# Kernel optimization log

Measured on AMD Instinct MI355X. Metric: run time of the kernel, lower is better.

Reference implementation:

```python
import jax, jax.numpy as jnp
import numpy as np

RES = 64            # resolution -> RES*RES grid points
BW = 0.3            # kernel bandwidth
P = 2.0             # weight power
BOX = np.array([[-3.0, 3.0], [-3.0, 3.0]], dtype=np.float32)  # fixed_box [[min,max],[min,max]]


def _grid():
    # regular RES x RES grid over BOX, flattened to (M, 2)
    ax0 = np.linspace(BOX[0, 0], BOX[0, 1], RES, dtype=np.float32)
    ax1 = np.linspace(BOX[1, 0], BOX[1, 1], RES, dtype=np.float32)
    g0, g1 = np.meshgrid(ax0, ax1, indexing='ij')
    return jnp.asarray(np.stack([g0.ravel(), g1.ravel()], axis=-1))


def setup_inputs() -> dict:
    key = jax.random.key(0)
    k1, k2 = jax.random.split(key)
    Bs = jax.random.normal(k1, (4, 128, 16, 2), dtype=jnp.float32)  # birth corners (S,N,nB,2)
    Ds = jax.random.normal(k2, (4, 128, 16, 2), dtype=jnp.float32)  # death corners (S,N,nD,2)
    return {"Bs": Bs, "Ds": Ds}


def reference(Bs, Ds):
    # Bs: (S,N,nB,2) birth corners (pad with +inf), Ds: (S,N,nD,2) death corners (pad with -inf)
    x = _grid()                      # (M,2) grid points, M = RES*RES
    x0, x1 = x[:, 0], x[:, 1]

    # --- interleaving weights: dI0 per interval ---
    # pairwise relu(D - B).min(coords) -> max over (nB,nD); inf -> 0
    pw = jnp.min(jax.nn.relu(Ds[:, :, None, :, :] - Bs[:, :, :, None, :]), axis=-1)  # (S,N,nB,nD)
    w = jnp.max(pw, axis=(-1, -2))                                                   # (S,N)
    w = jnp.where(jnp.isfinite(w), w, 0.0)

    # --- distance from grid points to intervals ---
    # birth: min_k max_d (B[k,d] - x[d]); computed as elementwise max of the 2 coords
    db = jnp.min(
        jnp.maximum(Bs[..., 0][:, :, None, :] - x0[None, None, :, None],
                    Bs[..., 1][:, :, None, :] - x1[None, None, :, None]),
        axis=-1)                                                                     # (S,N,M)
    # death: min_k max_d (x[d] - D[k,d])
    dd = jnp.min(
        jnp.maximum(x0[None, None, :, None] - Ds[..., 0][:, :, None, :],
                    x1[None, None, :, None] - Ds[..., 1][:, :, None, :]),
        axis=-1)                                                                     # (S,N,M)
    dist = jnp.maximum(db, dd)                                                       # (S,N,M)

    # --- gaussian kernel, unsigned: exp(-0.5*(relu(dist)/bw)^2) * w^p, summed over intervals ---
    k = jnp.exp(-0.5 * (jax.nn.relu(dist) / BW) ** 2)
    img = jnp.sum(k * (w ** P)[:, :, None], axis=1)                                  # (S, M)
    return img  # flat vector per sample, shape (S, RES*RES)
```

## Files before the change

kernel.cpp:

```cpp
#include <hip/hip_runtime.h>
#include <math.h>

#define RES   64
#define NPTS  (RES * RES)
#define NB    4
#define NN    128
#define NP    16

#define PTS_PER_BLK 32
#define NCHUNKS     8
#define NPER        (NN / NCHUNKS)

__global__ __launch_bounds__(256)
void w2_kernel(const float* __restrict__ Bs, const float* __restrict__ Ds,
               float* __restrict__ w2) {
    const int b  = blockIdx.x;
    const int t  = threadIdx.x;
    const int n  = t & 127;
    const int jh = t >> 7;

    const float* Bn = Bs + (size_t)(b * NN + n) * NP * 2;
    const float* Dn = Ds + (size_t)(b * NN + n) * NP * 2;

    float b0[NP], b1[NP];
    #pragma unroll
    for (int i = 0; i < NP; ++i) { b0[i] = Bn[2 * i]; b1[i] = Bn[2 * i + 1]; }

    float w = 0.0f;
    #pragma unroll
    for (int jj = 0; jj < NP / 2; ++jj) {
        const int j = jh * (NP / 2) + jj;
        const float d0 = Dn[2 * j];
        const float d1 = Dn[2 * j + 1];
        #pragma unroll
        for (int i = 0; i < NP; ++i) {
            float m = fminf(d0 - b0[i], d1 - b1[i]);
            w = fmaxf(w, fmaxf(m, 0.0f));
        }
    }

    __shared__ float wp[2][NN];
    wp[jh][n] = w;
    __syncthreads();
    if (t < NN) {
        float wv = fmaxf(wp[0][t], wp[1][t]);
        if (!isfinite(wv)) wv = 0.0f;
        w2[b * NN + t] = wv * wv;
    }
}

__global__ __launch_bounds__(256)
void img_kernel(const float* __restrict__ Bs, const float* __restrict__ Ds,
                const float* __restrict__ w2, float* __restrict__ out) {
    __shared__ float sB[NN * NP * 2];
    __shared__ float sD[NN * NP * 2];
    __shared__ float sW2[NN];
    __shared__ float psum[NCHUNKS][PTS_PER_BLK + 1];

    const int b    = blockIdx.x >> 7;
    const int pblk = blockIdx.x & 127;
    const int t    = threadIdx.x;

    const float4* gB = (const float4*)(Bs + (size_t)b * NN * NP * 2);
    const float4* gD = (const float4*)(Ds + (size_t)b * NN * NP * 2);
    float4* s4B = (float4*)sB;
    float4* s4D = (float4*)sD;
    #pragma unroll
    for (int k = 0; k < 4; ++k) {
        s4B[t + 256 * k] = gB[t + 256 * k];
        s4D[t + 256 * k] = gD[t + 256 * k];
    }
    if (t < NN) sW2[t] = w2[b * NN + t];
    __syncthreads();

    const int point = t & 31;
    const int chunk = t >> 5;
    const int p  = pblk * PTS_PER_BLK + point;
    const int i0 = p >> 6;
    const int i1 = p & 63;
    const float x0 = -3.0f + 6.0f * (float)i0 / 63.0f;
    const float x1 = -3.0f + 6.0f * (float)i1 / 63.0f;
    const float c  = -0.5f / (0.3f * 0.3f);

    float acc = 0.0f;
    #pragma unroll 2
    for (int nn = 0; nn < NPER; ++nn) {
        const int n = chunk * NPER + nn;
        const float* Bn = sB + n * NP * 2;
        const float* Dn = sD + n * NP * 2;
        float db = 1e30f, dd = 1e30f;
        #pragma unroll
        for (int i = 0; i < NP; ++i) {
            db = fminf(db, fmaxf(Bn[2 * i]     - x0, Bn[2 * i + 1] - x1));
            dd = fminf(dd, fmaxf(x0 - Dn[2 * i],     x1 - Dn[2 * i + 1]));
        }
        const float r = fmaxf(fmaxf(db, dd), 0.0f);
        acc = fmaf(__expf(c * r * r), sW2[n], acc);
    }

    psum[chunk][point] = acc;
    __syncthreads();
    if (t < PTS_PER_BLK) {
        float s = 0.0f;
        #pragma unroll
        for (int cc = 0; cc < NCHUNKS; ++cc) s += psum[cc][t];
        out[(size_t)b * NPTS + pblk * PTS_PER_BLK + t] = s;
    }
}

extern "C" void kernel_launch(void* const* d_in, const int* in_sizes, int n_in,
                              void* d_out, int out_size, void* d_ws, size_t ws_size,
                              hipStream_t stream) {
    const float* Bs = (const float*)d_in[0];
    const float* Ds = (const float*)d_in[1];
    float* out = (float*)d_out;
    float* w2  = (float*)d_ws;

    w2_kernel<<<dim3(NB), dim3(256), 0, stream>>>(Bs, Ds, w2);
    img_kernel<<<dim3(NB * (NPTS / PTS_PER_BLK)), dim3(256), 0, stream>>>(Bs, Ds, w2, out);
}
```

Baseline: 67.85 us.

## Register-block four grid points per thread with padded float4 LDS reads

Each thread in the image kernel now handles four consecutive grid points that share the same x0 coordinate, over 4 intervals instead of 16. The x0 terms are computed once per corner and reused across the four points. Corner data is stored in LDS with a padded stride of 36 floats and read as float4, which cuts LDS load count and bank conflicts. In exchange the partial-sum reduction grows from 8 to 32 chunks per point, and the kernel uses more registers for the per-point accumulators.

```diff
diff --git a/kernel.cpp b/kernel.cpp
--- a/kernel.cpp
+++ b/kernel.cpp
@@ -6,10 +6,9 @@
 #define NB    4
 #define NN    128
 #define NP    16
-
+#define STRIDE 36
 #define PTS_PER_BLK 32
-#define NCHUNKS     8
-#define NPER        (NN / NCHUNKS)
+#define NCHUNK 32
 
 __global__ __launch_bounds__(256)
 void w2_kernel(const float* __restrict__ Bs, const float* __restrict__ Ds,
@@ -52,10 +51,10 @@
 __global__ __launch_bounds__(256)
 void img_kernel(const float* __restrict__ Bs, const float* __restrict__ Ds,
                 const float* __restrict__ w2, float* __restrict__ out) {
-    __shared__ float sB[NN * NP * 2];
-    __shared__ float sD[NN * NP * 2];
+    __shared__ __align__(16) float sB[NN * STRIDE];
+    __shared__ __align__(16) float sD[NN * STRIDE];
     __shared__ float sW2[NN];
-    __shared__ float psum[NCHUNKS][PTS_PER_BLK + 1];
+    __shared__ float psum[NCHUNK][PTS_PER_BLK + 1];
 
     const int b    = blockIdx.x >> 7;
     const int pblk = blockIdx.x & 127;
@@ -63,47 +62,69 @@
 
     const float4* gB = (const float4*)(Bs + (size_t)b * NN * NP * 2);
     const float4* gD = (const float4*)(Ds + (size_t)b * NN * NP * 2);
-    float4* s4B = (float4*)sB;
-    float4* s4D = (float4*)sD;
     #pragma unroll
-    for (int k = 0; k < 4; ++k) {
-        s4B[t + 256 * k] = gB[t + 256 * k];
-        s4D[t + 256 * k] = gD[t + 256 * k];
+    for (int r = 0; r < 4; ++r) {
+        const int m   = t + 256 * r;
+        const int off = (m >> 3) * STRIDE + (m & 7) * 4;
+        *(float4*)(sB + off) = gB[m];
+        *(float4*)(sD + off) = gD[m];
     }
     if (t < NN) sW2[t] = w2[b * NN + t];
     __syncthreads();
 
-    const int point = t & 31;
-    const int chunk = t >> 5;
-    const int p  = pblk * PTS_PER_BLK + point;
-    const int i0 = p >> 6;
-    const int i1 = p & 63;
+    const int g  = t & 7;
+    const int c  = t >> 3;
+    const int p0 = pblk * PTS_PER_BLK + 4 * g;
+    const int i0 = p0 >> 6;
     const float x0 = -3.0f + 6.0f * (float)i0 / 63.0f;
-    const float x1 = -3.0f + 6.0f * (float)i1 / 63.0f;
-    const float c  = -0.5f / (0.3f * 0.3f);
+    float x1v[4];
+    #pragma unroll
+    for (int j = 0; j < 4; ++j)
+        x1v[j] = -3.0f + 6.0f * (float)((p0 + j) & 63) / 63.0f;
 
-    float acc = 0.0f;
-    #pragma unroll 2
-    for (int nn = 0; nn < NPER; ++nn) {
-        const int n = chunk * NPER + nn;
-        const float* Bn = sB + n * NP * 2;
-        const float* Dn = sD + n * NP * 2;
-        float db = 1e30f, dd = 1e30f;
+    const float cexp = -0.5f / (0.3f * 0.3f);
+    float acc[4] = {0.0f, 0.0f, 0.0f, 0.0f};
+
+    for (int k = 0; k < 4; ++k) {
+        const int n = c + 32 * k;
+        const float4* B4 = (const float4*)(sB + n * STRIDE);
+        const float4* D4 = (const float4*)(sD + n * STRIDE);
+        float db[4] = {1e30f, 1e30f, 1e30f, 1e30f};
+        float dd[4] = {1e30f, 1e30f, 1e30f, 1e30f};
         #pragma unroll
-        for (int i = 0; i < NP; ++i) {
-            db = fminf(db, fmaxf(Bn[2 * i]     - x0, Bn[2 * i + 1] - x1));
-            dd = fminf(dd, fmaxf(x0 - Dn[2 * i],     x1 - Dn[2 * i + 1]));
+        for (int q = 0; q < 8; ++q) {
+            const float4 fb = B4[q];
+            const float4 fd = D4[q];
+            float s  = fb.x - x0;
+            float sd = x0 - fd.x;
+            #pragma unroll
+            for (int j = 0; j < 4; ++j) {
+                db[j] = fminf(db[j], fmaxf(s,  fb.y - x1v[j]));
+                dd[j] = fminf(dd[j], fmaxf(sd, x1v[j] - fd.y));
+            }
+            s  = fb.z - x0;
+            sd = x0 - fd.z;
+            #pragma unroll
+            for (int j = 0; j < 4; ++j) {
+                db[j] = fminf(db[j], fmaxf(s,  fb.w - x1v[j]));
+                dd[j] = fminf(dd[j], fmaxf(sd, x1v[j] - fd.w));
+            }
         }
-        const float r = fmaxf(fmaxf(db, dd), 0.0f);
-        acc = fmaf(__expf(c * r * r), sW2[n], acc);
+        const float w2n = sW2[n];
+        #pragma unroll
+        for (int j = 0; j < 4; ++j) {
+            const float r = fmaxf(fmaxf(db[j], dd[j]), 0.0f);
+            acc[j] = fmaf(__expf(cexp * r * r), w2n, acc[j]);
+        }
     }
 
-    psum[chunk][point] = acc;
+    #pragma unroll
+    for (int j = 0; j < 4; ++j) psum[c][4 * g + j] = acc[j];
     __syncthreads();
     if (t < PTS_PER_BLK) {
         float s = 0.0f;
         #pragma unroll
-        for (int cc = 0; cc < NCHUNKS; ++cc) s += psum[cc][t];
+        for (int q = 0; q < NCHUNK; ++q) s += psum[q][t];
         out[(size_t)b * NPTS + pblk * PTS_PER_BLK + t] = s;
     }
 }
```

Result: faster. 63.88 us (-5.8%).
